# Performance work log

Hardware: AMD Instinct MI355X
Metric: run time of the kernel (lower is better)

## Reference

```python
import jax, jax.numpy as jnp
import numpy as np

INNER_LR = 0.01


def setup_inputs() -> dict:
    key = jax.random.key(0)
    k1, k2, k3 = jax.random.split(key, 3)
    B, S, D = 4, 2048, 1024
    Ds = D // 4
    x = jax.random.normal(k1, (B, S, D), dtype=jnp.float32)
    W_down = jax.random.normal(k2, (D, Ds), dtype=jnp.float32) * (1.0 / np.sqrt(D))
    b_down = jnp.zeros((Ds,), dtype=jnp.float32)
    W_up = jax.random.normal(k3, (Ds, D), dtype=jnp.float32) * (1.0 / np.sqrt(Ds))
    b_up = jnp.zeros((D,), dtype=jnp.float32)
    return {"x": x, "W_down": W_down, "b_down": b_down, "W_up": W_up, "b_up": b_up}


def reference(x, W_down, b_down, W_up, b_up):
    B, S, D = x.shape
    Ds = D // 4
    # proj_down for all timesteps at once (batched GEMM): (B,S,Ds)
    feat = jnp.einsum('bsd,de->bse', x, W_down) + b_down

    def step(W_state, f_t):
        # f_t: (B,Ds); W_state: (B,Ds,Ds)
        pred = jnp.einsum('bi,bij->bj', f_t, W_state)        # (B,Ds)
        err = pred - f_t
        # outer-product gradient of reconstruction loss
        W_new = W_state - INNER_LR * jnp.einsum('bi,bj->bij', f_t, err)
        return W_new, pred

    W0 = jnp.zeros((B, Ds, Ds), dtype=x.dtype)
    _, preds = jax.lax.scan(step, W0, jnp.swapaxes(feat, 0, 1))  # preds: (S,B,Ds)
    preds = jnp.swapaxes(preds, 0, 1)                            # (B,S,Ds)
    # proj_up + residual, batched over all timesteps
    out = jnp.einsum('bse,ed->bsd', preds, W_up) + b_up + x
    return out
```

## Files before the change

kernel.cpp:

```cpp
#include <hip/hip_runtime.h>

#define LR 0.01f

constexpr int Bc  = 4;
constexpr int Sc  = 2048;
constexpr int Dc  = 1024;
constexpr int Dsc = 256;

typedef unsigned short u16;
typedef __attribute__((ext_vector_type(8))) short bf16x8;
typedef __attribute__((ext_vector_type(4))) float f32x4;

__device__ __forceinline__ u16 f2bf(float f) {
  unsigned u = __float_as_uint(f);
  unsigned r = (u + 0x7fff + ((u >> 16) & 1)) >> 16;
  return (u16)r;
}
__device__ __forceinline__ float bf2f(u16 h) {
  return __uint_as_float((unsigned)h << 16);
}

__device__ __forceinline__ void async_cp16(const void* g, void* l) {
  __builtin_amdgcn_global_load_lds(
      (const __attribute__((address_space(1))) unsigned int*)g,
      (__attribute__((address_space(3))) unsigned int*)l, 16, 0, 0);
}


__global__ __launch_bounds__(256) void gemm_bias(
    const float* __restrict__ A, const float* __restrict__ Bm,
    const float* __restrict__ bias, const float* __restrict__ resid,
    float* __restrict__ C, int M, int N, int K) {
  constexpr int BM = 64, BN = 64, BK = 16;
  __shared__ float As[BM][BK + 4];
  __shared__ float Bs[BK][BN + 4];

  const int bm = blockIdx.x * BM;
  const int bn = blockIdx.y * BN;
  const int tx = threadIdx.x & 15;
  const int ty = threadIdx.x >> 4;

  float acc[4][4] = {};

  for (int k0 = 0; k0 < K; k0 += BK) {
#pragma unroll
    for (int qq = 0; qq < 4; ++qq) {
      int m = ty + 16 * qq;
      As[m][tx] = A[(size_t)(bm + m) * K + k0 + tx];
    }
#pragma unroll
    for (int qq = 0; qq < 4; ++qq) {
      int i = threadIdx.x + 256 * qq;
      int k = i >> 6, n = i & 63;
      Bs[k][n] = Bm[(size_t)(k0 + k) * N + bn + n];
    }
    __syncthreads();
#pragma unroll
    for (int k4 = 0; k4 < BK; k4 += 4) {
      float4 a0 = *(const float4*)&As[ty * 4 + 0][k4];
      float4 a1 = *(const float4*)&As[ty * 4 + 1][k4];
      float4 a2 = *(const float4*)&As[ty * 4 + 2][k4];
      float4 a3 = *(const float4*)&As[ty * 4 + 3][k4];
      float4 b0 = *(const float4*)&Bs[k4 + 0][tx * 4];
      float4 b1 = *(const float4*)&Bs[k4 + 1][tx * 4];
      float4 b2 = *(const float4*)&Bs[k4 + 2][tx * 4];
      float4 b3 = *(const float4*)&Bs[k4 + 3][tx * 4];
#define ROWI(AI)                                          \
      acc[AI][0] = fmaf(a##AI.x, b0.x, acc[AI][0]);       \
      acc[AI][1] = fmaf(a##AI.x, b0.y, acc[AI][1]);       \
      acc[AI][2] = fmaf(a##AI.x, b0.z, acc[AI][2]);       \
      acc[AI][3] = fmaf(a##AI.x, b0.w, acc[AI][3]);       \
      acc[AI][0] = fmaf(a##AI.y, b1.x, acc[AI][0]);       \
      acc[AI][1] = fmaf(a##AI.y, b1.y, acc[AI][1]);       \
      acc[AI][2] = fmaf(a##AI.y, b1.z, acc[AI][2]);       \
      acc[AI][3] = fmaf(a##AI.y, b1.w, acc[AI][3]);       \
      acc[AI][0] = fmaf(a##AI.z, b2.x, acc[AI][0]);       \
      acc[AI][1] = fmaf(a##AI.z, b2.y, acc[AI][1]);       \
      acc[AI][2] = fmaf(a##AI.z, b2.z, acc[AI][2]);       \
      acc[AI][3] = fmaf(a##AI.z, b2.w, acc[AI][3]);       \
      acc[AI][0] = fmaf(a##AI.w, b3.x, acc[AI][0]);       \
      acc[AI][1] = fmaf(a##AI.w, b3.y, acc[AI][1]);       \
      acc[AI][2] = fmaf(a##AI.w, b3.z, acc[AI][2]);       \
      acc[AI][3] = fmaf(a##AI.w, b3.w, acc[AI][3]);
      ROWI(0) ROWI(1) ROWI(2) ROWI(3)
#undef ROWI
    }
    __syncthreads();
  }

  float4 bias4 = *(const float4*)&bias[bn + tx * 4];
#pragma unroll
  for (int i = 0; i < 4; ++i) {
    int m = bm + ty * 4 + i;
    float4 v;
    v.x = acc[i][0] + bias4.x;
    v.y = acc[i][1] + bias4.y;
    v.z = acc[i][2] + bias4.z;
    v.w = acc[i][3] + bias4.w;
    if (resid) {
      float4 r = *(const float4*)&resid[(size_t)m * N + bn + tx * 4];
      v.x += r.x; v.y += r.y; v.z += r.z; v.w += r.w;
    }
    *(float4*)&C[(size_t)m * N + bn + tx * 4] = v;
  }
}

__global__ __launch_bounds__(256) void castT_bf16(const float* __restrict__ W,
                                                  u16* __restrict__ WT,
                                                  int K, int N) {
  __shared__ float t[32][33];
  const int bk = blockIdx.x * 32, bn = blockIdx.y * 32;
  const int tx = threadIdx.x & 31, ty = threadIdx.x >> 5;
  for (int r = ty; r < 32; r += 8) t[r][tx] = W[(size_t)(bk + r) * N + bn + tx];
  __syncthreads();
  for (int r = ty; r < 32; r += 8)
    WT[(size_t)(bn + r) * K + bk + tx] = f2bf(t[tx][r]);
}

__global__ __launch_bounds__(256) void gemm_bf16_split(
    const u16* __restrict__ Ahi, const u16* __restrict__ Alo,
    const u16* __restrict__ BT, const float* __restrict__ bias,
    const float* __restrict__ resid, float* __restrict__ C,
    int M, int N, int K) {
  constexpr int BM = 64, BN = 64, BK = 32;
  __shared__ u16 sAh[2][BM * BK];
  __shared__ u16 sAl[2][BM * BK];
  __shared__ u16 sB[2][BN * BK];

  const int wv = threadIdx.x >> 6, lane = threadIdx.x & 63;
  const int bm = blockIdx.x * BM, bn = blockIdx.y * BN;
  const int qm = (wv >> 1) * 32, qn = (wv & 1) * 32;
  const int lr = lane & 15, lk = lane >> 4;

  const int srow = lane >> 2;
  const int skp  = (lane & 3) * 8;
  const int NKS = K / BK;

#define GSTAGE(BUF, KS)                                                   \
  {                                                                       \
    async_cp16(Ahi + (size_t)(bm + wv * 16 + srow) * K + (KS)*BK + skp,   \
               &sAh[BUF][wv * 512]);                                      \
    async_cp16(Alo + (size_t)(bm + wv * 16 + srow) * K + (KS)*BK + skp,   \
               &sAl[BUF][wv * 512]);                                      \
    async_cp16(BT + (size_t)(bn + wv * 16 + srow) * K + (KS)*BK + skp,    \
               &sB[BUF][wv * 512]);                                       \
  }

  f32x4 acc00 = {0.f, 0.f, 0.f, 0.f}, acc01 = {0.f, 0.f, 0.f, 0.f};
  f32x4 acc10 = {0.f, 0.f, 0.f, 0.f}, acc11 = {0.f, 0.f, 0.f, 0.f};

  GSTAGE(0, 0);
  GSTAGE(1, 1);
  asm volatile("s_waitcnt vmcnt(3)" ::: "memory");
  __builtin_amdgcn_s_barrier();

  for (int ks = 0; ks < NKS; ++ks) {
    const int cb = ks & 1;
    const u16* pAh = &sAh[cb][0];
    const u16* pAl = &sAl[cb][0];
    const u16* pB  = &sB[cb][0];
    bf16x8 ah0 = *(const bf16x8*)&pAh[(qm + lr) * BK + lk * 8];
    bf16x8 ah1 = *(const bf16x8*)&pAh[(qm + 16 + lr) * BK + lk * 8];
    bf16x8 al0 = *(const bf16x8*)&pAl[(qm + lr) * BK + lk * 8];
    bf16x8 al1 = *(const bf16x8*)&pAl[(qm + 16 + lr) * BK + lk * 8];
    bf16x8 b0  = *(const bf16x8*)&pB[(qn + lr) * BK + lk * 8];
    bf16x8 b1  = *(const bf16x8*)&pB[(qn + 16 + lr) * BK + lk * 8];
    acc00 = __builtin_amdgcn_mfma_f32_16x16x32_bf16(ah0, b0, acc00, 0, 0, 0);
    acc01 = __builtin_amdgcn_mfma_f32_16x16x32_bf16(ah0, b1, acc01, 0, 0, 0);
    acc10 = __builtin_amdgcn_mfma_f32_16x16x32_bf16(ah1, b0, acc10, 0, 0, 0);
    acc11 = __builtin_amdgcn_mfma_f32_16x16x32_bf16(ah1, b1, acc11, 0, 0, 0);
    acc00 = __builtin_amdgcn_mfma_f32_16x16x32_bf16(al0, b0, acc00, 0, 0, 0);
    acc01 = __builtin_amdgcn_mfma_f32_16x16x32_bf16(al0, b1, acc01, 0, 0, 0);
    acc10 = __builtin_amdgcn_mfma_f32_16x16x32_bf16(al1, b0, acc10, 0, 0, 0);
    acc11 = __builtin_amdgcn_mfma_f32_16x16x32_bf16(al1, b1, acc11, 0, 0, 0);
    __builtin_amdgcn_s_barrier();
    if (ks + 2 < NKS) {
      GSTAGE(cb, ks + 2);
      asm volatile("s_waitcnt vmcnt(3)" ::: "memory");
    } else {
      asm volatile("s_waitcnt vmcnt(0)" ::: "memory");
    }
    __builtin_amdgcn_s_barrier();
  }

#define WRT(ACC, AR, BC)                                                 \
  {                                                                      \
    _Pragma("unroll")                                                    \
    for (int r = 0; r < 4; ++r) {                                        \
      int row = bm + qm + (AR) + lk * 4 + r;                             \
      int col = bn + qn + (BC) + lr;                                     \
      float v = ACC[r] + bias[col];                                      \
      if (resid) v += resid[(size_t)row * N + col];                      \
      C[(size_t)row * N + col] = v;                                      \
    }                                                                    \
  }
  WRT(acc00, 0, 0) WRT(acc01, 0, 16) WRT(acc10, 16, 0) WRT(acc11, 16, 16)
#undef WRT
#undef GSTAGE
}


template <int CTRL, int RM>
__device__ __forceinline__ float dpp_sum(float v) {
  int moved = __builtin_amdgcn_update_dpp(0, __float_as_int(v), CTRL, RM, 0xF, false);
  return v + __int_as_float(moved);
}

__device__ __forceinline__ float rdlane(float v, int l) {
  return __int_as_float(__builtin_amdgcn_readlane(__float_as_int(v), l));
}

constexpr int RCH = 32;
constexpr int NCH = Sc / RCH;

__global__ __launch_bounds__(256) void gram_inv(const float* __restrict__ feat,
                                                float* __restrict__ MTg) {
  const int bc = blockIdx.x;
  __shared__ float Fl[32 * 260];
  __shared__ float Gl[32 * 32];
  __shared__ float Ml[32 * 32];
  const float* src = feat + (size_t)bc * RCH * Dsc;
  for (int i = threadIdx.x; i < 32 * 256; i += 256) {
    int r = i >> 8, cc = i & 255;
    Fl[r * 260 + cc] = src[i];
  }
  __syncthreads();
#pragma unroll
  for (int k2 = 0; k2 < 4; ++k2) {
    int idx = threadIdx.x + (k2 << 8);
    int t = idx >> 5, s = idx & 31;
    float sum = 0.f;
    if (s < t) {
      const float4* ft = (const float4*)&Fl[t * 260];
      const float4* fs = (const float4*)&Fl[s * 260];
#pragma unroll
      for (int i = 0; i < 64; ++i) {
        float4 a = ft[i], b = fs[i];
        sum = fmaf(a.x, b.x, sum); sum = fmaf(a.y, b.y, sum);
        sum = fmaf(a.z, b.z, sum); sum = fmaf(a.w, b.w, sum);
      }
      sum *= LR;
    }
    Gl[idx] = sum;
  }
  __syncthreads();
  if (threadIdx.x < 32) {
    const int s = threadIdx.x;
    for (int t = 0; t < 32; ++t) {
      float sum = 0.f;
      for (int u = 0; u < t; ++u)
        sum = fmaf(Gl[t * 32 + u], Ml[u * 32 + s], sum);
      Ml[t * 32 + s] = ((t == s) ? 1.f : 0.f) - sum;
    }
  }
  __syncthreads();
  float* dst = MTg + (size_t)bc * 1024;
#pragma unroll
  for (int k2 = 0; k2 < 4; ++k2) {
    int idx = threadIdx.x + (k2 << 8);
    int s = idx >> 5, t = idx & 31;
    dst[idx] = Ml[t * 32 + s];
  }
}

__device__ __forceinline__ void async_copy16f(const float* g, float* l) {
  __builtin_amdgcn_global_load_lds(
      (const __attribute__((address_space(1))) unsigned int*)g,
      (__attribute__((address_space(3))) unsigned int*)l, 16, 0, 0);
}

#define QROWS(X) X(0) X(1) X(2) X(3) X(4) X(5) X(6) X(7)

__global__ __launch_bounds__(512, 4) void ttt_scan(
    const float* __restrict__ feat, const float* __restrict__ MTg,
    u16* __restrict__ predsHi, u16* __restrict__ predsLo) {
  const int lane = threadIdx.x & 63;
  const int wv   = threadIdx.x >> 6;
  const int lm   = lane & 31;
  const int cl   = wv & 1;
  const int qr   = wv >> 1;
  const int rbase = qr << 3;

  const int bi  = blockIdx.x;
  const int xcd = bi & 7;
  const int b   = xcd >> 1;
  const int q   = ((bi >> 3) << 1) | (xcd & 1);
  const int j   = (q << 1) | cl;

  __shared__ float  ldsF[2][RCH * Dsc];
  __shared__ float  ldsE[2][4][64];
  __shared__ float4 ldsA[2][4][64];
  __shared__ float4 ldsW[2][64];

  const float* fb0 = feat + (size_t)b * Sc * Dsc;
  const float* Mg  = MTg + (size_t)b * NCH * 1024;
  u16* pbh = predsHi + (size_t)b * Sc * Dsc + j;
  u16* pbl = predsLo + (size_t)b * Sc * Dsc + j;

#define STAGE(BUF, C0)                                                     \
  {                                                                        \
    _Pragma("unroll")                                                      \
    for (int r_ = 0; r_ < 4; ++r_) {                                       \
      const int row_ = (wv << 2) | r_;                                     \
      async_copy16f(fb0 + (size_t)((C0) * RCH + row_) * Dsc + (lane << 2), \
                    &ldsF[BUF][row_ * Dsc]);                               \
    }                                                                      \
  }

#define LOADM(C1)                                          \
  {                                                        \
    const float* mp_ = Mg + (size_t)(C1) * 1024 + lm;      \
    Mn0 = mp_[(rbase + 0) * 32]; Mn1 = mp_[(rbase + 1) * 32]; \
    Mn2 = mp_[(rbase + 2) * 32]; Mn3 = mp_[(rbase + 3) * 32]; \
    Mn4 = mp_[(rbase + 4) * 32]; Mn5 = mp_[(rbase + 5) * 32]; \
    Mn6 = mp_[(rbase + 6) * 32]; Mn7 = mp_[(rbase + 7) * 32]; \
  }

#define DECLF(R) float4 F4_##R;
#define DECLD(R) float dsc_##R;

#define LOADF(R) F4_##R = *(const float4*)&pF2[(R) * 256 + (lane << 2)];

#define P0C(R)                                                                 \
  {                                                                            \
    float dd = fmaf(F4_##R.y, w4y, F4_##R.x * w4x) +                           \
               fmaf(F4_##R.w, w4w, F4_##R.z * w4z);                            \
    dd = dpp_sum<0x111, 0xF>(dd);                                              \
    dd = dpp_sum<0x112, 0xF>(dd);                                              \
    dd = dpp_sum<0x114, 0xF>(dd);                                              \
    dd = dpp_sum<0x118, 0xF>(dd);                                              \
    dd = dpp_sum<0x142, 0xA>(dd);                                              \
    dd = dpp_sum<0x143, 0xC>(dd);                                              \
    dsc_##R = rdlane(dd, 63);                                                  \
  }

#define MV(R) e_p = fmaf(Mc##R, dsc_##R, e_p);

#define ACCT(R)                                    \
  {                                                \
    float et_ = rdlane(v_e, rbase + (R));          \
    accx = fmaf(et_, F4_##R.x, accx);              \
    accy = fmaf(et_, F4_##R.y, accy);              \
    accz = fmaf(et_, F4_##R.z, accz);              \
    accw = fmaf(et_, F4_##R.w, accw);              \
  }

  float Mc0, Mc1, Mc2, Mc3, Mc4, Mc5, Mc6, Mc7;
  float Mn0, Mn1, Mn2, Mn3, Mn4, Mn5, Mn6, Mn7;

  STAGE(0, 0);
  STAGE(1, 1);
  LOADM(0);
  Mc0 = Mn0; Mc1 = Mn1; Mc2 = Mn2; Mc3 = Mn3;
  Mc4 = Mn4; Mc5 = Mn5; Mc6 = Mn6; Mc7 = Mn7;
  asm volatile("s_waitcnt vmcnt(12)" ::: "memory");
  __builtin_amdgcn_s_barrier();
  __builtin_amdgcn_sched_barrier(0);

  const int jl4 = j >> 2, jc = j & 3;
  float w4x = (lane == jl4 && jc == 0) ? -1.f : 0.f;
  float w4y = (lane == jl4 && jc == 1) ? -1.f : 0.f;
  float w4z = (lane == jl4 && jc == 2) ? -1.f : 0.f;
  float w4w = (lane == jl4 && jc == 3) ? -1.f : 0.f;

#pragma unroll 1
  for (int c = 0; c < NCH; ++c) {
    const int cb = c & 1;
    const float* pF  = &ldsF[cb][0];
    const float* pF2 = pF + (rbase << 8);

    if (c + 1 < NCH) LOADM(c + 1);

    QROWS(DECLF)
    QROWS(DECLD)
    float e_p = 0.f;
    float accx = 0.f, accy = 0.f, accz = 0.f, accw = 0.f;

    float v_fjcol = 0.f;
    if (qr == 0) v_fjcol = pF[lm * 256 + j];

    QROWS(LOADF)
    __builtin_amdgcn_sched_barrier(0);
    QROWS(P0C)

    MV(0) MV(1) MV(2) MV(3) MV(4) MV(5) MV(6) MV(7)

    ldsE[cl][qr][lane] = e_p;
    __builtin_amdgcn_s_barrier();
    float v_e = (ldsE[cl][0][lane] + ldsE[cl][1][lane]) +
                (ldsE[cl][2][lane] + ldsE[cl][3][lane]);

    if (qr == 0 && lane < 32) {
      float v = v_e + v_fjcol;
      u16 hi = f2bf(v);
      u16 lo = f2bf(v - bf2f(hi));
      pbh[(size_t)(c * RCH + lane) * Dsc] = hi;
      pbl[(size_t)(c * RCH + lane) * Dsc] = lo;
    }

    QROWS(ACCT)

    if (qr != 0) ldsA[cl][qr][lane] = make_float4(accx, accy, accz, accw);
    __builtin_amdgcn_s_barrier();
    if (qr == 0) {
      float4 a1 = ldsA[cl][1][lane], a2 = ldsA[cl][2][lane],
             a3 = ldsA[cl][3][lane];
      accx += a1.x + a2.x + a3.x; accy += a1.y + a2.y + a3.y;
      accz += a1.z + a2.z + a3.z; accw += a1.w + a2.w + a3.w;
      w4x = fmaf(-LR, accx, w4x); w4y = fmaf(-LR, accy, w4y);
      w4z = fmaf(-LR, accz, w4z); w4w = fmaf(-LR, accw, w4w);
      ldsW[cl][lane] = make_float4(w4x, w4y, w4z, w4w);
    }

    if (c + 2 < NCH) {
      STAGE(cb, c + 2);
      asm volatile("s_waitcnt vmcnt(12)" ::: "memory");
    } else {
      asm volatile("s_waitcnt vmcnt(0)" ::: "memory");
    }
    __builtin_amdgcn_s_barrier();
    if (qr != 0) {
      float4 wp = ldsW[cl][lane];
      w4x = wp.x; w4y = wp.y; w4z = wp.z; w4w = wp.w;
    }
    Mc0 = Mn0; Mc1 = Mn1; Mc2 = Mn2; Mc3 = Mn3;
    Mc4 = Mn4; Mc5 = Mn5; Mc6 = Mn6; Mc7 = Mn7;
    __builtin_amdgcn_sched_barrier(0);
  }
#undef ACCT
#undef MV
#undef P0C
#undef LOADF
#undef DECLD
#undef DECLF
#undef LOADM
#undef STAGE
}

extern "C" void kernel_launch(void* const* d_in, const int* in_sizes, int n_in,
                              void* d_out, int out_size, void* d_ws, size_t ws_size,
                              hipStream_t stream) {
  const float* x  = (const float*)d_in[0];
  const float* Wd = (const float*)d_in[1];
  const float* bd = (const float*)d_in[2];
  const float* Wu = (const float*)d_in[3];
  const float* bu = (const float*)d_in[4];
  float* out = (float*)d_out;

  const int M = Bc * Sc;

  float* feat    = (float*)d_ws;
  float* MTg     = feat + (size_t)Bc * Sc * Dsc;
  u16*   predsHi = (u16*)(MTg + (size_t)Bc * NCH * 1024);
  u16*   predsLo = predsHi + (size_t)Bc * Sc * Dsc;
  u16*   wuT     = predsLo + (size_t)Bc * Sc * Dsc;

  castT_bf16<<<dim3(Dsc / 32, Dc / 32), dim3(256), 0, stream>>>(
      Wu, wuT, Dsc, Dc);

  gemm_bias<<<dim3(M / 64, Dsc / 64), dim3(256), 0, stream>>>(
      x, Wd, bd, nullptr, feat, M, Dsc, Dc);

  gram_inv<<<dim3(Bc * NCH), dim3(256), 0, stream>>>(feat, MTg);

  ttt_scan<<<dim3(Bc * Dsc / 2), dim3(512), 0, stream>>>(
      feat, MTg, predsHi, predsLo);

  gemm_bf16_split<<<dim3(M / 64, Dc / 64), dim3(256), 0, stream>>>(
      predsHi, predsLo, wuT, bu, x, out, M, Dc, Dsc);
}
```

Before: 249.7 us.

## Replace FP32 down-projection GEMM with split-bf16 three-term MFMA GEMM

The scalar FP32 FMA GEMM for the down-projection is replaced by a bf16 MFMA GEMM that keeps near-FP32 accuracy by splitting x and W_down into hi/lo bf16 parts and summing three products (hi*hi, hi*lo, lo*hi). It adds a full pass that casts and splits x into two bf16 arrays, plus a transposed split of W_down. This trades extra memory traffic (about 32 MB written and read again) for moving the dominant compute onto matrix cores. The workspace is reorganised so the gram and preds buffers alias the x split buffers.

```diff
diff --git a/kernel.cpp b/kernel.cpp
--- a/kernel.cpp
+++ b/kernel.cpp
@@ -27,82 +27,18 @@
 }
 
 
-__global__ __launch_bounds__(256) void gemm_bias(
-    const float* __restrict__ A, const float* __restrict__ Bm,
-    const float* __restrict__ bias, const float* __restrict__ resid,
-    float* __restrict__ C, int M, int N, int K) {
-  constexpr int BM = 64, BN = 64, BK = 16;
-  __shared__ float As[BM][BK + 4];
-  __shared__ float Bs[BK][BN + 4];
-
-  const int bm = blockIdx.x * BM;
-  const int bn = blockIdx.y * BN;
-  const int tx = threadIdx.x & 15;
-  const int ty = threadIdx.x >> 4;
-
-  float acc[4][4] = {};
-
-  for (int k0 = 0; k0 < K; k0 += BK) {
-#pragma unroll
-    for (int qq = 0; qq < 4; ++qq) {
-      int m = ty + 16 * qq;
-      As[m][tx] = A[(size_t)(bm + m) * K + k0 + tx];
-    }
-#pragma unroll
-    for (int qq = 0; qq < 4; ++qq) {
-      int i = threadIdx.x + 256 * qq;
-      int k = i >> 6, n = i & 63;
-      Bs[k][n] = Bm[(size_t)(k0 + k) * N + bn + n];
-    }
-    __syncthreads();
-#pragma unroll
-    for (int k4 = 0; k4 < BK; k4 += 4) {
-      float4 a0 = *(const float4*)&As[ty * 4 + 0][k4];
-      float4 a1 = *(const float4*)&As[ty * 4 + 1][k4];
-      float4 a2 = *(const float4*)&As[ty * 4 + 2][k4];
-      float4 a3 = *(const float4*)&As[ty * 4 + 3][k4];
-      float4 b0 = *(const float4*)&Bs[k4 + 0][tx * 4];
-      float4 b1 = *(const float4*)&Bs[k4 + 1][tx * 4];
-      float4 b2 = *(const float4*)&Bs[k4 + 2][tx * 4];
-      float4 b3 = *(const float4*)&Bs[k4 + 3][tx * 4];
-#define ROWI(AI)                                          \
-      acc[AI][0] = fmaf(a##AI.x, b0.x, acc[AI][0]);       \
-      acc[AI][1] = fmaf(a##AI.x, b0.y, acc[AI][1]);       \
-      acc[AI][2] = fmaf(a##AI.x, b0.z, acc[AI][2]);       \
-      acc[AI][3] = fmaf(a##AI.x, b0.w, acc[AI][3]);       \
-      acc[AI][0] = fmaf(a##AI.y, b1.x, acc[AI][0]);       \
-      acc[AI][1] = fmaf(a##AI.y, b1.y, acc[AI][1]);       \
-      acc[AI][2] = fmaf(a##AI.y, b1.z, acc[AI][2]);       \
-      acc[AI][3] = fmaf(a##AI.y, b1.w, acc[AI][3]);       \
-      acc[AI][0] = fmaf(a##AI.z, b2.x, acc[AI][0]);       \
-      acc[AI][1] = fmaf(a##AI.z, b2.y, acc[AI][1]);       \
-      acc[AI][2] = fmaf(a##AI.z, b2.z, acc[AI][2]);       \
-      acc[AI][3] = fmaf(a##AI.z, b2.w, acc[AI][3]);       \
-      acc[AI][0] = fmaf(a##AI.w, b3.x, acc[AI][0]);       \
-      acc[AI][1] = fmaf(a##AI.w, b3.y, acc[AI][1]);       \
-      acc[AI][2] = fmaf(a##AI.w, b3.z, acc[AI][2]);       \
-      acc[AI][3] = fmaf(a##AI.w, b3.w, acc[AI][3]);
-      ROWI(0) ROWI(1) ROWI(2) ROWI(3)
-#undef ROWI
-    }
-    __syncthreads();
-  }
-
-  float4 bias4 = *(const float4*)&bias[bn + tx * 4];
-#pragma unroll
-  for (int i = 0; i < 4; ++i) {
-    int m = bm + ty * 4 + i;
-    float4 v;
-    v.x = acc[i][0] + bias4.x;
-    v.y = acc[i][1] + bias4.y;
-    v.z = acc[i][2] + bias4.z;
-    v.w = acc[i][3] + bias4.w;
-    if (resid) {
-      float4 r = *(const float4*)&resid[(size_t)m * N + bn + tx * 4];
-      v.x += r.x; v.y += r.y; v.z += r.z; v.w += r.w;
-    }
-    *(float4*)&C[(size_t)m * N + bn + tx * 4] = v;
-  }
+__global__ __launch_bounds__(256) void cast_split(const float* __restrict__ in,
+                                                  u16* __restrict__ hi,
+                                                  u16* __restrict__ lo) {
+  int i = (blockIdx.x * 256 + threadIdx.x) * 4;
+  float4 v = *(const float4*)&in[i];
+  ushort4 h, l;
+  h.x = f2bf(v.x); l.x = f2bf(v.x - bf2f(h.x));
+  h.y = f2bf(v.y); l.y = f2bf(v.y - bf2f(h.y));
+  h.z = f2bf(v.z); l.z = f2bf(v.z - bf2f(h.z));
+  h.w = f2bf(v.w); l.w = f2bf(v.w - bf2f(h.w));
+  *(ushort4*)&hi[i] = h;
+  *(ushort4*)&lo[i] = l;
 }
 
 __global__ __launch_bounds__(256) void castT_bf16(const float* __restrict__ W,
@@ -117,18 +53,121 @@
     WT[(size_t)(bn + r) * K + bk + tx] = f2bf(t[tx][r]);
 }
 
+__global__ __launch_bounds__(256) void castT_split(const float* __restrict__ W,
+                                                   u16* __restrict__ WThi,
+                                                   u16* __restrict__ WTlo,
+                                                   int K, int N) {
+  __shared__ float t[32][33];
+  const int bk = blockIdx.x * 32, bn = blockIdx.y * 32;
+  const int tx = threadIdx.x & 31, ty = threadIdx.x >> 5;
+  for (int r = ty; r < 32; r += 8) t[r][tx] = W[(size_t)(bk + r) * N + bn + tx];
+  __syncthreads();
+  for (int r = ty; r < 32; r += 8) {
+    float v = t[tx][r];
+    u16 h = f2bf(v);
+    WThi[(size_t)(bn + r) * K + bk + tx] = h;
+    WTlo[(size_t)(bn + r) * K + bk + tx] = f2bf(v - bf2f(h));
+  }
+}
+
+__global__ __launch_bounds__(256) void gemm_bf16_split3(
+    const u16* __restrict__ Ahi, const u16* __restrict__ Alo,
+    const u16* __restrict__ BThi, const u16* __restrict__ BTlo,
+    const float* __restrict__ bias, float* __restrict__ C,
+    int M, int N, int K) {
+  constexpr int BK = 32;
+  __shared__ u16 sAh[2][64 * BK];
+  __shared__ u16 sAl[2][64 * BK];
+  __shared__ u16 sBh[2][64 * BK];
+  __shared__ u16 sBl[2][64 * BK];
+
+  const int wv = threadIdx.x >> 6, lane = threadIdx.x & 63;
+  const int bm = blockIdx.x * 64, bn = blockIdx.y * 64;
+  const int qm = (wv >> 1) * 32, qn = (wv & 1) * 32;
+  const int lr = lane & 15, lk = lane >> 4;
+
+  const int srow = lane >> 2;
+  const int skp  = (lane & 3) * 8;
+  const int NKS = K / BK;
+
+#define GSTAGE(BUF, KS)                                                   \
+  {                                                                       \
+    async_cp16(Ahi + (size_t)(bm + wv * 16 + srow) * K + (KS)*BK + skp,   \
+               &sAh[BUF][wv * 512]);                                      \
+    async_cp16(Alo + (size_t)(bm + wv * 16 + srow) * K + (KS)*BK + skp,   \
+               &sAl[BUF][wv * 512]);                                      \
+    async_cp16(BThi + (size_t)(bn + wv * 16 + srow) * K + (KS)*BK + skp,  \
+               &sBh[BUF][wv * 512]);                                      \
+    async_cp16(BTlo + (size_t)(bn + wv * 16 + srow) * K + (KS)*BK + skp,  \
+               &sBl[BUF][wv * 512]);                                      \
+  }
+
+  f32x4 acc00 = {0.f, 0.f, 0.f, 0.f}, acc01 = {0.f, 0.f, 0.f, 0.f};
+  f32x4 acc10 = {0.f, 0.f, 0.f, 0.f}, acc11 = {0.f, 0.f, 0.f, 0.f};
+
+  GSTAGE(0, 0);
+  GSTAGE(1, 1);
+  asm volatile("s_waitcnt vmcnt(4)" ::: "memory");
+  __builtin_amdgcn_s_barrier();
+
+  for (int ks = 0; ks < NKS; ++ks) {
+    const int cb = ks & 1;
+    bf16x8 ah0 = *(const bf16x8*)&sAh[cb][(qm + lr) * BK + lk * 8];
+    bf16x8 ah1 = *(const bf16x8*)&sAh[cb][(qm + 16 + lr) * BK + lk * 8];
+    bf16x8 al0 = *(const bf16x8*)&sAl[cb][(qm + lr) * BK + lk * 8];
+    bf16x8 al1 = *(const bf16x8*)&sAl[cb][(qm + 16 + lr) * BK + lk * 8];
+    bf16x8 bh0 = *(const bf16x8*)&sBh[cb][(qn + lr) * BK + lk * 8];
+    bf16x8 bh1 = *(const bf16x8*)&sBh[cb][(qn + 16 + lr) * BK + lk * 8];
+    bf16x8 bl0 = *(const bf16x8*)&sBl[cb][(qn + lr) * BK + lk * 8];
+    bf16x8 bl1 = *(const bf16x8*)&sBl[cb][(qn + 16 + lr) * BK + lk * 8];
+    acc00 = __builtin_amdgcn_mfma_f32_16x16x32_bf16(ah0, bh0, acc00, 0, 0, 0);
+    acc01 = __builtin_amdgcn_mfma_f32_16x16x32_bf16(ah0, bh1, acc01, 0, 0, 0);
+    acc10 = __builtin_amdgcn_mfma_f32_16x16x32_bf16(ah1, bh0, acc10, 0, 0, 0);
+    acc11 = __builtin_amdgcn_mfma_f32_16x16x32_bf16(ah1, bh1, acc11, 0, 0, 0);
+    acc00 = __builtin_amdgcn_mfma_f32_16x16x32_bf16(ah0, bl0, acc00, 0, 0, 0);
+    acc01 = __builtin_amdgcn_mfma_f32_16x16x32_bf16(ah0, bl1, acc01, 0, 0, 0);
+    acc10 = __builtin_amdgcn_mfma_f32_16x16x32_bf16(ah1, bl0, acc10, 0, 0, 0);
+    acc11 = __builtin_amdgcn_mfma_f32_16x16x32_bf16(ah1, bl1, acc11, 0, 0, 0);
+    acc00 = __builtin_amdgcn_mfma_f32_16x16x32_bf16(al0, bh0, acc00, 0, 0, 0);
+    acc01 = __builtin_amdgcn_mfma_f32_16x16x32_bf16(al0, bh1, acc01, 0, 0, 0);
+    acc10 = __builtin_amdgcn_mfma_f32_16x16x32_bf16(al1, bh0, acc10, 0, 0, 0);
+    acc11 = __builtin_amdgcn_mfma_f32_16x16x32_bf16(al1, bh1, acc11, 0, 0, 0);
+    __builtin_amdgcn_s_barrier();
+    if (ks + 2 < NKS) {
+      GSTAGE(cb, ks + 2);
+      asm volatile("s_waitcnt vmcnt(4)" ::: "memory");
+    } else {
+      asm volatile("s_waitcnt vmcnt(0)" ::: "memory");
+    }
+    __builtin_amdgcn_s_barrier();
+  }
+
+#define WRT(ACC, AR, BC)                                                 \
+  {                                                                      \
+    _Pragma("unroll")                                                    \
+    for (int r = 0; r < 4; ++r) {                                        \
+      int row = bm + qm + (AR) + lk * 4 + r;                             \
+      int col = bn + qn + (BC) + lr;                                     \
+      C[(size_t)row * N + col] = ACC[r] + bias[col];                     \
+    }                                                                    \
+  }
+  WRT(acc00, 0, 0) WRT(acc01, 0, 16) WRT(acc10, 16, 0) WRT(acc11, 16, 16)
+#undef WRT
+#undef GSTAGE
+}
+
 __global__ __launch_bounds__(256) void gemm_bf16_split(
     const u16* __restrict__ Ahi, const u16* __restrict__ Alo,
     const u16* __restrict__ BT, const float* __restrict__ bias,
     const float* __restrict__ resid, float* __restrict__ C,
     int M, int N, int K) {
-  constexpr int BM = 64, BN = 64, BK = 32;
-  __shared__ u16 sAh[2][BM * BK];
-  __shared__ u16 sAl[2][BM * BK];
-  __shared__ u16 sB[2][BN * BK];
+  constexpr int BK = 32;
+  __shared__ u16 sAh[2][64 * BK];
+  __shared__ u16 sAl[2][64 * BK];
+  __shared__ u16 sB[2][64 * BK];
 
   const int wv = threadIdx.x >> 6, lane = threadIdx.x & 63;
-  const int bm = blockIdx.x * BM, bn = blockIdx.y * BN;
+  const int bm = blockIdx.x * 64, bn = blockIdx.y * 64;
   const int qm = (wv >> 1) * 32, qn = (wv & 1) * 32;
   const int lr = lane & 15, lk = lane >> 4;
 
@@ -156,15 +195,12 @@
 
   for (int ks = 0; ks < NKS; ++ks) {
     const int cb = ks & 1;
-    const u16* pAh = &sAh[cb][0];
-    const u16* pAl = &sAl[cb][0];
-    const u16* pB  = &sB[cb][0];
-    bf16x8 ah0 = *(const bf16x8*)&pAh[(qm + lr) * BK + lk * 8];
-    bf16x8 ah1 = *(const bf16x8*)&pAh[(qm + 16 + lr) * BK + lk * 8];
-    bf16x8 al0 = *(const bf16x8*)&pAl[(qm + lr) * BK + lk * 8];
-    bf16x8 al1 = *(const bf16x8*)&pAl[(qm + 16 + lr) * BK + lk * 8];
-    bf16x8 b0  = *(const bf16x8*)&pB[(qn + lr) * BK + lk * 8];
-    bf16x8 b1  = *(const bf16x8*)&pB[(qn + 16 + lr) * BK + lk * 8];
+    bf16x8 ah0 = *(const bf16x8*)&sAh[cb][(qm + lr) * BK + lk * 8];
+    bf16x8 ah1 = *(const bf16x8*)&sAh[cb][(qm + 16 + lr) * BK + lk * 8];
+    bf16x8 al0 = *(const bf16x8*)&sAl[cb][(qm + lr) * BK + lk * 8];
+    bf16x8 al1 = *(const bf16x8*)&sAl[cb][(qm + 16 + lr) * BK + lk * 8];
+    bf16x8 b0  = *(const bf16x8*)&sB[cb][(qn + lr) * BK + lk * 8];
+    bf16x8 b1  = *(const bf16x8*)&sB[cb][(qn + 16 + lr) * BK + lk * 8];
     acc00 = __builtin_amdgcn_mfma_f32_16x16x32_bf16(ah0, b0, acc00, 0, 0, 0);
     acc01 = __builtin_amdgcn_mfma_f32_16x16x32_bf16(ah0, b1, acc01, 0, 0, 0);
     acc10 = __builtin_amdgcn_mfma_f32_16x16x32_bf16(ah1, b0, acc10, 0, 0, 0);
@@ -449,17 +485,24 @@
 
   const int M = Bc * Sc;
 
-  float* feat    = (float*)d_ws;
-  float* MTg     = feat + (size_t)Bc * Sc * Dsc;
+  u16*   xhi   = (u16*)d_ws;
+  u16*   xlo   = xhi + (size_t)M * Dc;
+  float* feat  = (float*)(xlo + (size_t)M * Dc);
+  u16*   wdThi = (u16*)(feat + (size_t)M * Dsc);
+  u16*   wdTlo = wdThi + (size_t)Dc * Dsc;
+  u16*   wuT   = wdTlo + (size_t)Dc * Dsc;
+  float* MTg     = (float*)xhi;
   u16*   predsHi = (u16*)(MTg + (size_t)Bc * NCH * 1024);
   u16*   predsLo = predsHi + (size_t)Bc * Sc * Dsc;
-  u16*   wuT     = predsLo + (size_t)Bc * Sc * Dsc;
-
+
+  cast_split<<<dim3(M * Dc / 1024), dim3(256), 0, stream>>>(x, xhi, xlo);
+  castT_split<<<dim3(Dc / 32, Dsc / 32), dim3(256), 0, stream>>>(
+      Wd, wdThi, wdTlo, Dc, Dsc);
   castT_bf16<<<dim3(Dsc / 32, Dc / 32), dim3(256), 0, stream>>>(
       Wu, wuT, Dsc, Dc);
 
-  gemm_bias<<<dim3(M / 64, Dsc / 64), dim3(256), 0, stream>>>(
-      x, Wd, bd, nullptr, feat, M, Dsc, Dc);
+  gemm_bf16_split3<<<dim3(M / 64, Dsc / 64), dim3(256), 0, stream>>>(
+      xhi, xlo, wdThi, wdTlo, bd, feat, M, Dsc, Dc);
 
   gram_inv<<<dim3(Bc * NCH), dim3(256), 0, stream>>>(feat, MTg);
 
```

Measured after the change: 213.3 us. -14.6%, faster.
